# Optimization experiments

Hardware: AMD Instinct MI355X
Metric: run time of the kernel (lower is better)

The kernel has to match this reference:

```python
import jax, jax.numpy as jnp
import numpy as np

# channels_choice from the module: [8,16,24,32,40,48,56,64]
CH = jnp.arange(8, 72, 8)
EPS = 1e-5

def _masks():
    # [8,64] binary masks: mask[i, ch] = 1 if ch < channels_choice[i]
    return (jnp.arange(64)[None, :] < CH[:, None]).astype(jnp.float32)

def _bn(x, axes):
    # BatchNorm, affine=False, track_running_stats=False -> batch statistics
    mu = jnp.mean(x, axes, keepdims=True)
    var = jnp.var(x, axes, keepdims=True)
    return (x - mu) * jax.lax.rsqrt(var + EPS)

def _conv3(x, w):
    return jax.lax.conv_general_dilated(x, w, (1, 1), 'SAME',
                                        dimension_numbers=('NCHW', 'OIHW', 'NCHW'))

def _nor_conv(x, w1, w2, a1, a2):
    # Entangled two-part nor_conv edge.
    # p1: relu -> conv3x3 -> bn, mixture over 8 output-channel widths. Slicing
    # output channels + zero-pad + alpha-weighted sum collapses (BN is per-channel)
    # to a soft channel mask m1.
    masks = _masks()                      # [8,64]
    m1 = masks.T @ a1                     # [64] soft output-channel mask
    h = _bn(_conv3(jax.nn.relu(x), w1), (0, 2, 3)) * m1[None, :, None, None]
    # p2: conv3x3 -> bn, mixture over 8 input-channel widths. BN is nonlinear, so
    # the 8 candidates are genuinely computed (vectorized on a leading axis).
    xs = h[None] * masks[:, None, :, None, None]   # [8,B,64,H,W]
    K, B, C, H, W = xs.shape
    y = _conv3(xs.reshape(K * B, C, H, W), w2).reshape(K, B, C, H, W)
    y = _bn(y, (1, 3, 4))
    return jnp.einsum('k,kbchw->bchw', a2, y)

def _avg_pool3(x):
    # AvgPool2d(3, stride=1, padding=1, count_include_pad=False)
    s = jax.lax.reduce_window(x, 0.0, jax.lax.add, (1, 1, 3, 3), (1, 1, 1, 1), 'SAME')
    cnt = jax.lax.reduce_window(jnp.ones((1, 1) + x.shape[2:], x.dtype), 0.0,
                                jax.lax.add, (1, 1, 3, 3), (1, 1, 1, 1), 'SAME')
    return s / cnt

def _combi_mask(a1, a2):
    # combi=True mixture over itertools.product(channels, channels) with weights
    # a1[i]*a2[j]; for channelwise ops (skip/pool) slicing in to c_i then out to c_j
    # keeps channels < min(c_i,c_j), so the double sum factorizes into m1*m2.
    masks = _masks()
    return (masks.T @ a1) * (masks.T @ a2)

def _cell(inputs, alphas1, alphas2, W1_0, W2_0, W1_1, W2_1, W1_4, W2_4, W1_5, W2_5):
    cm = _combi_mask(alphas1, alphas2)[None, :, None, None]
    # genotype: 1<-(conv~0) | 2<-(conv~0, avgpool~1) | 3<-(skip~0, conv~1, conv~2)
    n1 = _nor_conv(inputs, W1_0, W2_0, alphas1, alphas2)
    n2 = _nor_conv(inputs, W1_1, W2_1, alphas1, alphas2) + _avg_pool3(n1) * cm
    n3 = (inputs * cm
          + _nor_conv(n1, W1_4, W2_4, alphas1, alphas2)
          + _nor_conv(n2, W1_5, W2_5, alphas1, alphas2))
    return n3

def setup_inputs():
    key = jax.random.key(0)
    ks = jax.random.split(key, 12)
    B, C, H, W = 64, 64, 32, 32
    a1 = jax.random.uniform(ks[1], (8,), jnp.float32)
    a2 = jax.random.uniform(ks[2], (8,), jnp.float32)
    d = {
        'inputs': jax.random.normal(ks[0], (B, C, H, W), jnp.float32),
        'alphas1': a1 / a1.sum(),
        'alphas2': a2 / a2.sum(),
    }
    wscale = 0.05  # ~ 1/sqrt(64*9) fan-in init
    for i, name in enumerate(['W1_0', 'W2_0', 'W1_1', 'W2_1', 'W1_4', 'W2_4', 'W1_5', 'W2_5']):
        d[name] = jax.random.normal(ks[3 + i], (64, 64, 3, 3), jnp.float32) * wscale
    return d

def reference(inputs, alphas1, alphas2, W1_0, W2_0, W1_1, W2_1, W1_4, W2_4, W1_5, W2_5):
    return _cell(inputs, alphas1, alphas2, W1_0, W2_0, W1_1, W2_1, W1_4, W2_4, W1_5, W2_5)
```

## Files before the change

### kernel.cpp

```cpp
#include <hip/hip_runtime.h>

#define EPS 1e-5f
#define NRED 65536.0f
#define IMST 73984
#define PATCH 8704

typedef short bf16x8 __attribute__((ext_vector_type(8)));
typedef float f32x4 __attribute__((ext_vector_type(4)));
typedef unsigned short u16;

#define MFMA16(a, b, c) __builtin_amdgcn_mfma_f32_16x16x32_bf16(a, b, c, 0, 0, 0)
#define SWZ(px, oct) ((px) * 64 + (((oct) ^ ((px) & 7)) * 8))

__device__ __forceinline__ u16 f2bf(float x) {
  union { float f; unsigned u; } v; v.f = x;
  unsigned r = v.u + 0x7FFF + ((v.u >> 16) & 1);
  return (u16)(r >> 16);
}
__device__ __forceinline__ float bf2f(u16 h) {
  union { unsigned u; float f; } v; v.u = ((unsigned)h) << 16;
  return v.f;
}
__device__ __forceinline__ unsigned pk2(float a, float b) {
  return (unsigned)f2bf(a) | ((unsigned)f2bf(b) << 16);
}

template <int CTRL>
__device__ __forceinline__ float dpp_mov(float x) {
  int xi = __builtin_bit_cast(int, x);
  int r = __builtin_amdgcn_update_dpp(0, xi, CTRL, 0xF, 0xF, true);
  return __builtin_bit_cast(float, r);
}
__device__ __forceinline__ float row_reduce16(float x) {
  x += dpp_mov<0x111>(x);
  x += dpp_mov<0x112>(x);
  x += dpp_mov<0x114>(x);
  x += dpp_mov<0x118>(x);
  return x;
}

__device__ __forceinline__ void stage_mask(const u16* __restrict__ src,
                                           u16* __restrict__ shp, int tid, int R0) {
#pragma unroll
  for (int i = 0; i < 5; ++i) {
    int c = i * 256 + tid;
    if (i == 4 && tid >= 64) break;
    int px = c >> 3, oct = c & 7;
    int prow = px / 34, pcol = px - prow * 34;
    bool halo = (R0 + prow == 0) || (R0 + prow == 33) || (pcol == 0) || (pcol == 33);
    uint4 v = {0u, 0u, 0u, 0u};
    if (!halo) v = *(const uint4*)&src[(size_t)c * 8];
    *(uint4*)&shp[SWZ(px, oct)] = v;
  }
}

__device__ __forceinline__ void stage_affine(const u16* __restrict__ src,
                                             u16* __restrict__ shp, int tid, int R0,
                                             const float* __restrict__ stE) {
  const int oct0 = tid & 7;
  float s[8], bb[8];
#pragma unroll
  for (int j = 0; j < 8; ++j) { s[j] = stE[oct0 * 8 + j]; bb[j] = stE[64 + oct0 * 8 + j]; }
#pragma unroll
  for (int i = 0; i < 5; ++i) {
    int c = i * 256 + tid;
    if (i == 4 && tid >= 64) break;
    int px = c >> 3, oct = c & 7;
    int prow = px / 34, pcol = px - prow * 34;
    bool halo = (R0 + prow == 0) || (R0 + prow == 33) || (pcol == 0) || (pcol == 33);
    uint4 o = {0u, 0u, 0u, 0u};
    if (!halo) {
      uint4 u = *(const uint4*)&src[(size_t)c * 8];
      unsigned uv[4] = {u.x, u.y, u.z, u.w};
      unsigned rv[4];
#pragma unroll
      for (int p2 = 0; p2 < 4; ++p2) {
        float lo = bf2f((u16)(uv[p2] & 0xffff)) * s[p2 * 2] + bb[p2 * 2];
        float hi = bf2f((u16)(uv[p2] >> 16)) * s[p2 * 2 + 1] + bb[p2 * 2 + 1];
        rv[p2] = pk2(lo, hi);
      }
      o.x = rv[0]; o.y = rv[1]; o.z = rv[2]; o.w = rv[3];
    }
    *(uint4*)&shp[SWZ(px, oct)] = o;
  }
}


__global__ void pack_wT1_k(const float* __restrict__ w0, const float* __restrict__ w1,
                           const float* __restrict__ w2, const float* __restrict__ w3,
                           u16* __restrict__ wT1) {
  int e = blockIdx.x / 9, tap = blockIdx.x % 9;
  const float* w = e == 0 ? w0 : e == 1 ? w1 : e == 2 ? w2 : w3;
  u16* dst = wT1 + e * 36864 + tap * 4096;
  for (int idx = threadIdx.x; idx < 4096; idx += 256) {
    int co = idx >> 6, ci = idx & 63;
    dst[idx] = f2bf(w[(co * 64 + ci) * 9 + tap]);
  }
}

__global__ void pack_wG_k(const float* __restrict__ w0, const float* __restrict__ w1,
                          const float* __restrict__ w2, const float* __restrict__ w3,
                          u16* __restrict__ wG64, u16* __restrict__ wT8) {
  int e = blockIdx.y;
  const float* w = e == 0 ? w0 : e == 1 ? w1 : e == 2 ? w2 : w3;
  int bx = blockIdx.x;
  int g, tap;
  u16* dst;
  if (bx < 64) { g = bx >> 3; tap = bx & 7; dst = wG64 + e * 32768 + bx * 512; }
  else         { g = bx - 64; tap = 8;      dst = wT8 + e * 4096 + g * 512; }
  for (int idx = threadIdx.x; idx < 512; idx += 256) {
    int co = idx >> 3, cig = idx & 7;
    dst[idx] = f2bf(w[(co * 64 + g * 8 + cig) * 9 + tap]);
  }
}

__global__ __launch_bounds__(256) void transpose_k(const float* __restrict__ x,
                                                   u16* __restrict__ xT) {
  __shared__ __align__(16) u16 sh[64 * 72];
  const int tid = threadIdx.x;
  const int b = blockIdx.x >> 4, slab = blockIdx.x & 15;
  const int ln = tid & 63, w = tid >> 6;
  const float* xb = x + (size_t)b * 65536 + slab * 64;
#pragma unroll
  for (int i = 0; i < 16; ++i) {
    int ci = w + i * 4;
    float v = xb[ci * 1024 + ln];
    sh[ln * 72 + ci] = f2bf(fmaxf(v, 0.f));
  }
  __syncthreads();
  u16* dst = xT + (size_t)b * IMST;
#pragma unroll
  for (int j = 0; j < 2; ++j) {
    int idx = tid + j * 256;
    int p = idx >> 3, oct = idx & 7;
    int gp = slab * 64 + p;
    int R = gp >> 5, C = gp & 31;
    *(uint4*)&dst[((R + 1) * 34 + C + 1) * 64 + oct * 8] = *(const uint4*)&sh[p * 72 + oct * 8];
  }
}

__global__ void zero_halo_k(u16* __restrict__ buf) {
  int b = blockIdx.x, tid = threadIdx.x;
  if (tid >= 132) return;
  int R, C;
  if (tid < 34) { R = 0; C = tid; }
  else if (tid < 68) { R = 33; C = tid - 34; }
  else if (tid < 100) { R = tid - 67; C = 0; }
  else { R = tid - 99; C = 33; }
  u16* p = buf + (size_t)b * IMST + (size_t)(R * 34 + C) * 64;
  uint4 z = {0u, 0u, 0u, 0u};
#pragma unroll
  for (int i = 0; i < 8; ++i) *(uint4*)&p[i * 8] = z;
}

__global__ __launch_bounds__(256, 4) void convA_k(const u16* __restrict__ in0,
                                                  const u16* __restrict__ in1,
                                                  const u16* __restrict__ wTa,
                                                  const u16* __restrict__ wTb,
                                                  u16* __restrict__ t0,
                                                  u16* __restrict__ t1,
                                                  float* __restrict__ pA) {
  __shared__ __align__(16) u16 shp[PATCH];
  __shared__ float sA[64], qA[64];
  const int tid = threadIdx.x;
  const int b = blockIdx.y, R0 = blockIdx.x * 2, z = blockIdx.z;
  const u16* xin = z ? in1 : in0;
  const u16* wT = z ? wTb : wTa;
  u16* t = z ? t1 : t0;
  if (tid < 64) { sA[tid] = 0.f; qA[tid] = 0.f; }
  stage_mask(xin + (size_t)b * IMST + (size_t)R0 * 2176, shp, tid, R0);
  const int lane = tid & 63, w = tid >> 6;
  const int ln = lane & 15, quad = lane >> 4;
  const int lr = w >> 1, mh = w & 1;
  const u16* wbase = wT + (size_t)((mh * 2) * 16 + ln) * 64 + quad * 8;
  __syncthreads();
  f32x4 acc[2][2];
#pragma unroll
  for (int m2 = 0; m2 < 2; ++m2)
#pragma unroll
    for (int nf = 0; nf < 2; ++nf) acc[m2][nf] = (f32x4){0.f, 0.f, 0.f, 0.f};
#pragma unroll 3
  for (int tap = 0; tap < 9; ++tap) {
    const int dy = tap / 3, dx = tap % 3;
    const int px0 = (lr + dy) * 34 + ln + dx;
    bf16x8 A[2][2];
#pragma unroll
    for (int m2 = 0; m2 < 2; ++m2)
#pragma unroll
      for (int h = 0; h < 2; ++h)
        A[m2][h] = *(const bf16x8*)&wbase[(size_t)(tap * 64 + m2 * 16) * 64 + h * 32];
#pragma unroll
    for (int h = 0; h < 2; ++h) {
      const int oct = h * 4 + quad;
      bf16x8 b0 = *(const bf16x8*)&shp[SWZ(px0, oct)];
      bf16x8 b1 = *(const bf16x8*)&shp[SWZ(px0 + 16, oct)];
      acc[0][0] = MFMA16(A[0][h], b0, acc[0][0]);
      acc[0][1] = MFMA16(A[0][h], b1, acc[0][1]);
      acc[1][0] = MFMA16(A[1][h], b0, acc[1][0]);
      acc[1][1] = MFMA16(A[1][h], b1, acc[1][1]);
    }
  }
  const int R = R0 + lr;
#pragma unroll
  for (int m2 = 0; m2 < 2; ++m2) {
    const int cob = (mh * 2 + m2) * 16 + quad * 4;
#pragma unroll
    for (int nf = 0; nf < 2; ++nf) {
      u16* tb = t + (size_t)b * IMST + (size_t)((R + 1) * 34 + nf * 16 + ln + 1) * 64 + cob;
      uint2 pk;
      pk.x = pk2(acc[m2][nf][0], acc[m2][nf][1]);
      pk.y = pk2(acc[m2][nf][2], acc[m2][nf][3]);
      *(uint2*)tb = pk;
    }
#pragma unroll
    for (int r = 0; r < 4; ++r) {
      float v0 = acc[m2][0][r], v1 = acc[m2][1][r];
      float s = row_reduce16(v0) + row_reduce16(v1);
      float q = row_reduce16(v0 * v0) + row_reduce16(v1 * v1);
      if (ln == 15) {
        atomicAdd(&sA[cob + r], s);
        atomicAdd(&qA[cob + r], q);
      }
    }
  }
  __syncthreads();
  const int blk = z * 1024 + blockIdx.y * 16 + blockIdx.x;
  if (tid < 64) pA[blk * 128 + tid] = sA[tid];
  else if (tid < 128) pA[blk * 128 + tid] = qA[tid - 64];
}

__global__ __launch_bounds__(256) void reducerA_k(const float* __restrict__ pA,
                                                  const float* __restrict__ a1,
                                                  float* __restrict__ stBase) {
  const int tid = threadIdx.x, c = blockIdx.x, z = blockIdx.y;
  const float* pAe = pA + (size_t)z * 1024 * 128;
  float s = 0.f, q = 0.f;
  for (int i = tid; i < 1024; i += 256) {
    s += pAe[i * 128 + c];
    q += pAe[i * 128 + 64 + c];
  }
#pragma unroll
  for (int off = 32; off; off >>= 1) { s += __shfl_xor(s, off); q += __shfl_xor(q, off); }
  __shared__ float red[8];
  int wv = tid >> 6;
  if ((tid & 63) == 0) { red[wv] = s; red[4 + wv] = q; }
  __syncthreads();
  if (tid == 0) {
    float S = red[0] + red[1] + red[2] + red[3];
    float Q = red[4] + red[5] + red[6] + red[7];
    int g = c >> 3;
    float m = 0.f;
    for (int i = g; i < 8; ++i) m += a1[i];
    float mu = S * (1.f / NRED);
    float var = Q * (1.f / NRED) - mu * mu;
    float r = rsqrtf(var + EPS);
    float* stE = stBase + z * 2048;
    stE[c] = r * m;
    stE[64 + c] = -mu * r * m;
  }
}

__global__ __launch_bounds__(256, 4) void convC_k(const u16* __restrict__ t0,
                                                  const u16* __restrict__ t1,
                                                  const u16* __restrict__ wG64,
                                                  const u16* __restrict__ wT8,
                                                  const float* __restrict__ stBase,
                                                  float* __restrict__ pC) {
  __shared__ __align__(16) u16 shp[PATCH];
  __shared__ __align__(16) u16 shA[64 * 16 * 8];
  __shared__ __align__(16) u16 shA2[8 * 16 * 8];
  __shared__ float sC[4][128], qC[4][128];
  const int tid = threadIdx.x;
  const int b = blockIdx.y, R0 = blockIdx.x * 2;
  const int edge = blockIdx.z;
  const u16* t = edge ? t1 : t0;
  const float* stE = stBase + edge * 2048;
  const u16* wGe = wG64 + edge * 32768;
  const u16* wT8e = wT8 + edge * 4096;
  {
    float* scf = (float*)sC;
    float* qcf = (float*)qC;
#pragma unroll
    for (int i = 0; i < 2; ++i) { scf[i * 256 + tid] = 0.f; qcf[i * 256 + tid] = 0.f; }
  }
  stage_affine(t + (size_t)b * IMST + (size_t)R0 * 2176, shp, tid, R0, stE);
#pragma unroll
  for (int i = 0; i < 4; ++i) {
    int c = i * 256 + tid;
    int row = c >> 4, col = c & 15;
    *(uint4*)&shA[c * 8] = *(const uint4*)&wGe[(size_t)(row * 64 + col) * 8];
  }
  if (tid < 128) {
    int g = tid >> 4, col = tid & 15;
    *(uint4*)&shA2[tid * 8] = *(const uint4*)&wT8e[(size_t)(g * 64 + col) * 8];
  }
  __syncthreads();
  const int lane = tid & 63, w = tid >> 6;
  const int ln = lane & 15, quad = lane >> 4;
  const int lrow = w >> 1, colbase = (w & 1) * 16;
  int px[3];
#pragma unroll
  for (int ch = 0; ch < 3; ++ch) {
    int tp = ch * 4 + quad; if (tp > 8) tp = 8;
    px[ch] = (lrow + tp / 3) * 34 + colbase + ln + tp % 3;
  }
#pragma unroll 1
  for (int coq = 0; coq < 4; ++coq) {
    f32x4 acc[8];
#pragma unroll
    for (int g = 0; g < 8; ++g) acc[g] = (f32x4){0.f, 0.f, 0.f, 0.f};
#pragma unroll
    for (int g = 0; g < 8; ++g) {
#pragma unroll
      for (int ch = 0; ch < 3; ++ch) {
        bf16x8 bx = *(const bf16x8*)&shp[SWZ(px[ch], g)];
        bf16x8 aw;
        if (ch < 2) {
          aw = *(const bf16x8*)&shA[((g * 8 + ch * 4 + quad) * 16 + ln) * 8];
        } else {
          aw = (bf16x8){0, 0, 0, 0, 0, 0, 0, 0};
          if (quad == 0) aw = *(const bf16x8*)&shA2[(g * 16 + ln) * 8];
        }
        acc[g] = MFMA16(aw, bx, acc[g]);
      }
    }
    f32x4 P = (f32x4){0.f, 0.f, 0.f, 0.f};
#pragma unroll
    for (int k = 0; k < 8; ++k) {
      P += acc[k];
#pragma unroll
      for (int r = 0; r < 4; ++r) {
        float v = P[r];
        float s = row_reduce16(v);
        float q = row_reduce16(v * v);
        if (ln == 15) {
          atomicAdd(&sC[coq][k * 16 + quad * 4 + r], s);
          atomicAdd(&qC[coq][k * 16 + quad * 4 + r], q);
        }
      }
    }
    __syncthreads();
    if (coq < 3) {
      const int nq = coq + 1;
#pragma unroll
      for (int i = 0; i < 4; ++i) {
        int c = i * 256 + tid;
        int row = c >> 4, col = c & 15;
        *(uint4*)&shA[c * 8] = *(const uint4*)&wGe[(size_t)(row * 64 + nq * 16 + col) * 8];
      }
      if (tid < 128) {
        int g = tid >> 4, col = tid & 15;
        *(uint4*)&shA2[tid * 8] = *(const uint4*)&wT8e[(size_t)(g * 64 + nq * 16 + col) * 8];
      }
      __syncthreads();
    }
  }
  const int blk = blockIdx.y * 16 + blockIdx.x;
#pragma unroll 1
  for (int coq = 0; coq < 4; ++coq) {
    const size_t base = ((size_t)(edge * 4 + coq) * 1024 + blk) * 256;
    if (tid < 128) pC[base + tid] = sC[coq][tid];
    else pC[base + 128 + (tid - 128)] = qC[coq][tid - 128];
  }
}

__global__ __launch_bounds__(256) void redCprepE_k(const float* __restrict__ pC,
                                                   const float* __restrict__ w2a,
                                                   const float* __restrict__ w2b,
                                                   const float* __restrict__ a1,
                                                   const float* __restrict__ a2,
                                                   float* __restrict__ stBase,
                                                   u16* __restrict__ wEbase,
                                                   float* __restrict__ cm) {
  const int tid = threadIdx.x, c = blockIdx.x, z = blockIdx.y;
  const int coq = c >> 4, cl = c & 15;
  const float* w2 = z ? w2b : w2a;
  float* stE = stBase + z * 2048;
  u16* wE = wEbase + z * 36864;
  float s[8], q[8];
#pragma unroll
  for (int k = 0; k < 8; ++k) { s[k] = 0.f; q[k] = 0.f; }
  for (int i = tid; i < 1024; i += 256) {
    const float* pb = pC + ((size_t)(z * 4 + coq) * 1024 + i) * 256;
#pragma unroll
    for (int k = 0; k < 8; ++k) {
      s[k] += pb[k * 16 + cl];
      q[k] += pb[128 + k * 16 + cl];
    }
  }
#pragma unroll
  for (int k = 0; k < 8; ++k) {
#pragma unroll
    for (int off = 32; off; off >>= 1) { s[k] += __shfl_xor(s[k], off); q[k] += __shfl_xor(q[k], off); }
  }
  __shared__ float red[4][16];
  __shared__ float gL[8];
  int wv = tid >> 6;
  if ((tid & 63) == 0) {
#pragma unroll
    for (int k = 0; k < 8; ++k) { red[wv][k * 2] = s[k]; red[wv][k * 2 + 1] = q[k]; }
  }
  __syncthreads();
  if (tid == 0) {
    float suf = 0.f, bias = 0.f;
    for (int k = 7; k >= 0; --k) {
      float S = red[0][k * 2] + red[1][k * 2] + red[2][k * 2] + red[3][k * 2];
      float Q = red[0][k * 2 + 1] + red[1][k * 2 + 1] + red[2][k * 2 + 1] + red[3][k * 2 + 1];
      float mu = S * (1.f / NRED);
      float var = Q * (1.f / NRED) - mu * mu;
      float rr = rsqrtf(var + EPS);
      bias -= a2[k] * mu * rr;
      suf += a2[k] * rr;
      gL[k] = suf;
    }
    stE[128 + c] = bias;
    if (z == 0) {
      int g = c >> 3;
      float m1 = 0.f, m2 = 0.f;
      for (int i = g; i < 8; ++i) { m1 += a1[i]; m2 += a2[i]; }
      cm[c] = m1 * m2;
    }
  }
  __syncthreads();
  for (int idx = tid; idx < 576; idx += 256) {
    int tap = idx >> 6, ci = idx & 63;
    wE[(tap * 64 + c) * 64 + ci] = f2bf(w2[(c * 64 + ci) * 9 + tap] * gL[ci >> 3]);
  }
}

template <int MODE>
__global__ __launch_bounds__(256, 4) void convE_k(const u16* __restrict__ t,
                                                  const float* __restrict__ stE,
                                                  const u16* __restrict__ wEp,
                                                  u16* __restrict__ d1,
                                                  u16* __restrict__ d2,
                                                  const float* __restrict__ cm) {
  __shared__ __align__(16) u16 shp[PATCH];
  __shared__ float cmL[64], biasL[64];
  const int tid = threadIdx.x;
  const int b = blockIdx.y, R0 = blockIdx.x * 2;
  if (tid < 64) { cmL[tid] = cm[tid]; biasL[tid] = stE[128 + tid]; }
  stage_affine(t + (size_t)b * IMST + (size_t)R0 * 2176, shp, tid, R0, stE);
  const int lane = tid & 63, w = tid >> 6;
  const int ln = lane & 15, quad = lane >> 4;
  const int lr = w >> 1, mh = w & 1;
  const u16* wbase = wEp + (size_t)((mh * 2) * 16 + ln) * 64 + quad * 8;
  __syncthreads();
  f32x4 acc[2][2];
#pragma unroll
  for (int m2 = 0; m2 < 2; ++m2)
#pragma unroll
    for (int nf = 0; nf < 2; ++nf) acc[m2][nf] = (f32x4){0.f, 0.f, 0.f, 0.f};
#pragma unroll 3
  for (int tap = 0; tap < 9; ++tap) {
    const int dy = tap / 3, dx = tap % 3;
    const int px0 = (lr + dy) * 34 + ln + dx;
    bf16x8 A[2][2];
#pragma unroll
    for (int m2 = 0; m2 < 2; ++m2)
#pragma unroll
      for (int h = 0; h < 2; ++h)
        A[m2][h] = *(const bf16x8*)&wbase[(size_t)(tap * 64 + m2 * 16) * 64 + h * 32];
#pragma unroll
    for (int h = 0; h < 2; ++h) {
      const int oct = h * 4 + quad;
      bf16x8 b0 = *(const bf16x8*)&shp[SWZ(px0, oct)];
      bf16x8 b1 = *(const bf16x8*)&shp[SWZ(px0 + 16, oct)];
      acc[0][0] = MFMA16(A[0][h], b0, acc[0][0]);
      acc[0][1] = MFMA16(A[0][h], b1, acc[0][1]);
      acc[1][0] = MFMA16(A[1][h], b0, acc[1][0]);
      acc[1][1] = MFMA16(A[1][h], b1, acc[1][1]);
    }
  }
  const int R = R0 + lr;
#pragma unroll
  for (int m2 = 0; m2 < 2; ++m2) {
    const int cob = (mh * 2 + m2) * 16 + quad * 4;
#pragma unroll
    for (int nf = 0; nf < 2; ++nf) {
      const int C = nf * 16 + ln;
      const size_t haloPx = (size_t)b * IMST + (size_t)((R + 1) * 34 + C + 1) * 64 + cob;
      float v[4];
#pragma unroll
      for (int r = 0; r < 4; ++r) v[r] = acc[m2][nf][r] + biasL[cob + r];
      if (MODE == 0) {
        uint2 pk, pkr;
        pk.x = pk2(v[0], v[1]); pk.y = pk2(v[2], v[3]);
        pkr.x = pk2(fmaxf(v[0], 0.f), fmaxf(v[1], 0.f));
        pkr.y = pk2(fmaxf(v[2], 0.f), fmaxf(v[3], 0.f));
        *(uint2*)&d1[haloPx] = pk;
        *(uint2*)&d2[haloPx] = pkr;
      } else {
        float ps[4] = {0.f, 0.f, 0.f, 0.f};
        const size_t pb2 = (size_t)b * IMST + (size_t)(R * 34 + C) * 64 + cob;
#pragma unroll
        for (int dy = 0; dy < 3; ++dy)
#pragma unroll
          for (int dx = 0; dx < 3; ++dx) {
            uint2 u = *(const uint2*)&d2[pb2 + (size_t)(dy * 34 + dx) * 64];
            ps[0] += bf2f((u16)(u.x & 0xffff));
            ps[1] += bf2f((u16)(u.x >> 16));
            ps[2] += bf2f((u16)(u.y & 0xffff));
            ps[3] += bf2f((u16)(u.y >> 16));
          }
        float rows = 3.f - (R == 0 ? 1.f : 0.f) - (R == 31 ? 1.f : 0.f);
        float cols = 3.f - (C == 0 ? 1.f : 0.f) - (C == 31 ? 1.f : 0.f);
        float inv = 1.f / (rows * cols);
        uint2 pkr;
        float t0v = fmaxf(v[0] + ps[0] * inv * cmL[cob], 0.f);
        float t1v = fmaxf(v[1] + ps[1] * inv * cmL[cob + 1], 0.f);
        float t2v = fmaxf(v[2] + ps[2] * inv * cmL[cob + 2], 0.f);
        float t3v = fmaxf(v[3] + ps[3] * inv * cmL[cob + 3], 0.f);
        pkr.x = pk2(t0v, t1v); pkr.y = pk2(t2v, t3v);
        *(uint2*)&d1[haloPx] = pkr;
      }
    }
  }
}

__global__ __launch_bounds__(256, 4) void convE23_k(const u16* __restrict__ t0,
                                                    const u16* __restrict__ t1,
                                                    const float* __restrict__ stBase,
                                                    const u16* __restrict__ wE2,
                                                    const u16* __restrict__ wE3,
                                                    float* __restrict__ outp,
                                                    const float* __restrict__ x,
                                                    const float* __restrict__ cm) {
  __shared__ __align__(16) u16 shp2[2 * PATCH];
  __shared__ float cmL[64], biasL[64];
  const int tid = threadIdx.x;
  const int b = blockIdx.y, R0 = blockIdx.x * 2;
  if (tid < 64) {
    cmL[tid] = cm[tid];
    biasL[tid] = stBase[128 + tid] + stBase[2048 + 128 + tid];
  }
  stage_affine(t0 + (size_t)b * IMST + (size_t)R0 * 2176, shp2, tid, R0, stBase);
  stage_affine(t1 + (size_t)b * IMST + (size_t)R0 * 2176, shp2 + PATCH, tid, R0, stBase + 2048);
  __syncthreads();
  const int lane = tid & 63, w = tid >> 6;
  const int ln = lane & 15, quad = lane >> 4;
  const int lr = w >> 1, mh = w & 1;
  f32x4 acc[2][2];
#pragma unroll
  for (int m2 = 0; m2 < 2; ++m2)
#pragma unroll
    for (int nf = 0; nf < 2; ++nf) acc[m2][nf] = (f32x4){0.f, 0.f, 0.f, 0.f};
#pragma unroll 1
  for (int ei = 0; ei < 2; ++ei) {
    const u16* wEp = ei ? wE3 : wE2;
    const u16* sp = &shp2[ei * PATCH];
    const u16* wbase = wEp + (size_t)((mh * 2) * 16 + ln) * 64 + quad * 8;
#pragma unroll 3
    for (int tap = 0; tap < 9; ++tap) {
      const int dy = tap / 3, dx = tap % 3;
      const int px0 = (lr + dy) * 34 + ln + dx;
      bf16x8 A[2][2];
#pragma unroll
      for (int m2 = 0; m2 < 2; ++m2)
#pragma unroll
        for (int h = 0; h < 2; ++h)
          A[m2][h] = *(const bf16x8*)&wbase[(size_t)(tap * 64 + m2 * 16) * 64 + h * 32];
#pragma unroll
      for (int h = 0; h < 2; ++h) {
        const int oct = h * 4 + quad;
        bf16x8 b0 = *(const bf16x8*)&sp[SWZ(px0, oct)];
        bf16x8 b1 = *(const bf16x8*)&sp[SWZ(px0 + 16, oct)];
        acc[0][0] = MFMA16(A[0][h], b0, acc[0][0]);
        acc[0][1] = MFMA16(A[0][h], b1, acc[0][1]);
        acc[1][0] = MFMA16(A[1][h], b0, acc[1][0]);
        acc[1][1] = MFMA16(A[1][h], b1, acc[1][1]);
      }
    }
  }
  const int R = R0 + lr;
#pragma unroll
  for (int m2 = 0; m2 < 2; ++m2) {
    const int cob = (mh * 2 + m2) * 16 + quad * 4;
#pragma unroll
    for (int nf = 0; nf < 2; ++nf) {
      const int C = nf * 16 + ln;
      size_t base = (size_t)b * 65536 + (size_t)cob * 1024 + R * 32 + C;
#pragma unroll
      for (int r = 0; r < 4; ++r)
        outp[base + (size_t)r * 1024] =
            acc[m2][nf][r] + biasL[cob + r] + x[base + (size_t)r * 1024] * cmL[cob + r];
    }
  }
}

extern "C" void kernel_launch(void* const* d_in, const int* in_sizes, int n_in,
                              void* d_out, int out_size, void* d_ws, size_t ws_size,
                              hipStream_t stream) {
  const float* x  = (const float*)d_in[0];
  const float* a1 = (const float*)d_in[1];
  const float* a2 = (const float*)d_in[2];
  const float* W1[4] = {(const float*)d_in[3], (const float*)d_in[5],
                        (const float*)d_in[7], (const float*)d_in[9]};
  const float* W2[4] = {(const float*)d_in[4], (const float*)d_in[6],
                        (const float*)d_in[8], (const float*)d_in[10]};
  float* out = (float*)d_out;
  char* ws = (char*)d_ws;
  const size_t HB = (size_t)IMST * 64 * 2;
  u16* xT  = (u16*)ws;
  u16* t0  = (u16*)(ws + HB);
  u16* t1  = (u16*)(ws + 2 * HB);
  u16* n1T = (u16*)(ws + 3 * HB);
  u16* n1r = (u16*)(ws + 4 * HB);
  u16* n2r = (u16*)(ws + 5 * HB);
  char* p = ws + 6 * HB;
  float* st  = (float*)p;            p += 8256 * 4;
  u16* wT1   = (u16*)p;              p += 4 * 36864 * 2;
  u16* wG64  = (u16*)p;              p += 4 * 32768 * 2;
  u16* wT8   = (u16*)p;              p += 4 * 4096 * 2;
  u16* wE    = (u16*)p;              p += 4 * 36864 * 2;
  float* pA  = (float*)p;            p += 2 * 1024 * 128 * 4;
  float* pC  = (float*)p;
  float* cm  = st + 8192;

  pack_wT1_k<<<36, 256, 0, stream>>>(W1[0], W1[1], W1[2], W1[3], wT1);
  pack_wG_k<<<dim3(72, 4), 256, 0, stream>>>(W2[0], W2[1], W2[2], W2[3], wG64, wT8);
  transpose_k<<<1024, 256, 0, stream>>>(x, xT);
  zero_halo_k<<<64, 160, 0, stream>>>(n1T);

  dim3 gA(16, 64, 2), gC(16, 64, 2), gE(16, 64);
  convA_k<<<gA, 256, 0, stream>>>(xT, xT, wT1, wT1 + 36864, t0, t1, pA);
  reducerA_k<<<dim3(64, 2), 256, 0, stream>>>(pA, a1, st);
  convC_k<<<gC, 256, 0, stream>>>(t0, t1, wG64, wT8, st, pC);
  redCprepE_k<<<dim3(64, 2), 256, 0, stream>>>(pC, W2[0], W2[1], a1, a2, st, wE, cm);
  convE_k<0><<<gE, 256, 0, stream>>>(t0, st, wE, n1T, n1r, cm);
  convE_k<1><<<gE, 256, 0, stream>>>(t1, st + 2048, wE + 36864, n2r, n1T, cm);
  convA_k<<<gA, 256, 0, stream>>>(n1r, n2r, wT1 + 2 * 36864, wT1 + 3 * 36864, t0, t1, pA);
  reducerA_k<<<dim3(64, 2), 256, 0, stream>>>(pA, a1, st + 4096);
  convC_k<<<gC, 256, 0, stream>>>(t0, t1, wG64 + 2 * 32768, wT8 + 2 * 4096, st + 4096, pC);
  redCprepE_k<<<dim3(64, 2), 256, 0, stream>>>(pC, W2[2], W2[3], a1, a2, st + 4096,
                                               wE + 2 * 36864, cm);
  convE23_k<<<gE, 256, 0, stream>>>(t0, t1, st + 4096, wE + 2 * 36864, wE + 3 * 36864,
                                    out, x, cm);
}
```

Baseline: 463.5 us.

## Enlarge convC tile to four rows with 512 threads and prefetch next weights

convC now runs 512-thread blocks, each covering four output rows instead of two, so every block stages a six-row patch and halves the grid. Each staged weight quarter is reused across twice as many pixels. The next output-channel quarter's weights are loaded into registers before the MFMA loop and written to shared memory afterward, hiding global load latency. The partial-stat buffer and its reducer shrink to 512 blocks per edge. The cost is higher register and LDS pressure per block, and the launch bound asks for 6 blocks of 512 threads, which may not be achievable.

Result: no change. 458.6 us (-1.1%).

```diff
diff --git a/kernel.cpp b/kernel.cpp
--- a/kernel.cpp
+++ b/kernel.cpp
@@ -4,6 +4,7 @@
 #define NRED 65536.0f
 #define IMST 73984
 #define PATCH 8704
+#define PATCH6 13056
 
 typedef short bf16x8 __attribute__((ext_vector_type(8)));
 typedef float f32x4 __attribute__((ext_vector_type(4)));
@@ -260,33 +261,57 @@
   }
 }
 
-__global__ __launch_bounds__(256, 4) void convC_k(const u16* __restrict__ t0,
+__global__ __launch_bounds__(512, 6) void convC_k(const u16* __restrict__ t0,
                                                   const u16* __restrict__ t1,
                                                   const u16* __restrict__ wG64,
                                                   const u16* __restrict__ wT8,
                                                   const float* __restrict__ stBase,
                                                   float* __restrict__ pC) {
-  __shared__ __align__(16) u16 shp[PATCH];
+  __shared__ __align__(16) u16 shp[PATCH6];
   __shared__ __align__(16) u16 shA[64 * 16 * 8];
   __shared__ __align__(16) u16 shA2[8 * 16 * 8];
   __shared__ float sC[4][128], qC[4][128];
   const int tid = threadIdx.x;
-  const int b = blockIdx.y, R0 = blockIdx.x * 2;
+  const int b = blockIdx.y, R0 = blockIdx.x * 4;
   const int edge = blockIdx.z;
   const u16* t = edge ? t1 : t0;
   const float* stE = stBase + edge * 2048;
   const u16* wGe = wG64 + edge * 32768;
   const u16* wT8e = wT8 + edge * 4096;
+  ((float*)sC)[tid] = 0.f;
+  ((float*)qC)[tid] = 0.f;
   {
-    float* scf = (float*)sC;
-    float* qcf = (float*)qC;
-#pragma unroll
-    for (int i = 0; i < 2; ++i) { scf[i * 256 + tid] = 0.f; qcf[i * 256 + tid] = 0.f; }
-  }
-  stage_affine(t + (size_t)b * IMST + (size_t)R0 * 2176, shp, tid, R0, stE);
-#pragma unroll
-  for (int i = 0; i < 4; ++i) {
-    int c = i * 256 + tid;
+    const int oct0 = tid & 7;
+    float sc[8], bc[8];
+#pragma unroll
+    for (int j = 0; j < 8; ++j) { sc[j] = stE[oct0 * 8 + j]; bc[j] = stE[64 + oct0 * 8 + j]; }
+    const u16* src = t + (size_t)b * IMST + (size_t)R0 * 2176;
+#pragma unroll
+    for (int i = 0; i < 4; ++i) {
+      int c = i * 512 + tid;
+      if (i == 3 && tid >= 96) break;
+      int px = c >> 3, oct = c & 7;
+      int prow = px / 34, pcol = px - prow * 34;
+      bool halo = (R0 + prow == 0) || (R0 + prow == 33) || (pcol == 0) || (pcol == 33);
+      uint4 o = {0u, 0u, 0u, 0u};
+      if (!halo) {
+        uint4 u = *(const uint4*)&src[(size_t)c * 8];
+        unsigned uv[4] = {u.x, u.y, u.z, u.w};
+        unsigned rv[4];
+#pragma unroll
+        for (int p2 = 0; p2 < 4; ++p2) {
+          float lo = bf2f((u16)(uv[p2] & 0xffff)) * sc[p2 * 2] + bc[p2 * 2];
+          float hi = bf2f((u16)(uv[p2] >> 16)) * sc[p2 * 2 + 1] + bc[p2 * 2 + 1];
+          rv[p2] = pk2(lo, hi);
+        }
+        o.x = rv[0]; o.y = rv[1]; o.z = rv[2]; o.w = rv[3];
+      }
+      *(uint4*)&shp[SWZ(px, oct)] = o;
+    }
+  }
+#pragma unroll
+  for (int i = 0; i < 2; ++i) {
+    int c = i * 512 + tid;
     int row = c >> 4, col = c & 15;
     *(uint4*)&shA[c * 8] = *(const uint4*)&wGe[(size_t)(row * 64 + col) * 8];
   }
@@ -306,6 +331,20 @@
   }
 #pragma unroll 1
   for (int coq = 0; coq < 4; ++coq) {
+    uint4 wr0, wr1, wr2;
+    if (coq < 3) {
+      const int nq = coq + 1;
+      {
+        int c = tid;
+        wr0 = *(const uint4*)&wGe[(size_t)((c >> 4) * 64 + nq * 16 + (c & 15)) * 8];
+      }
+      {
+        int c = 512 + tid;
+        wr1 = *(const uint4*)&wGe[(size_t)((c >> 4) * 64 + nq * 16 + (c & 15)) * 8];
+      }
+      if (tid < 128)
+        wr2 = *(const uint4*)&wT8e[(size_t)((tid >> 4) * 64 + nq * 16 + (tid & 15)) * 8];
+    }
     f32x4 acc[8];
 #pragma unroll
     for (int g = 0; g < 8; ++g) acc[g] = (f32x4){0.f, 0.f, 0.f, 0.f};
@@ -341,26 +380,19 @@
     }
     __syncthreads();
     if (coq < 3) {
-      const int nq = coq + 1;
-#pragma unroll
-      for (int i = 0; i < 4; ++i) {
-        int c = i * 256 + tid;
-        int row = c >> 4, col = c & 15;
-        *(uint4*)&shA[c * 8] = *(const uint4*)&wGe[(size_t)(row * 64 + nq * 16 + col) * 8];
-      }
-      if (tid < 128) {
-        int g = tid >> 4, col = tid & 15;
-        *(uint4*)&shA2[tid * 8] = *(const uint4*)&wT8e[(size_t)(g * 64 + nq * 16 + col) * 8];
-      }
+      *(uint4*)&shA[(size_t)tid * 8] = wr0;
+      *(uint4*)&shA[(size_t)(512 + tid) * 8] = wr1;
+      if (tid < 128) *(uint4*)&shA2[tid * 8] = wr2;
       __syncthreads();
     }
   }
-  const int blk = blockIdx.y * 16 + blockIdx.x;
+  __syncthreads();
+  const int blk = blockIdx.y * 8 + blockIdx.x;
 #pragma unroll 1
   for (int coq = 0; coq < 4; ++coq) {
-    const size_t base = ((size_t)(edge * 4 + coq) * 1024 + blk) * 256;
+    const size_t base = ((size_t)(edge * 4 + coq) * 512 + blk) * 256;
     if (tid < 128) pC[base + tid] = sC[coq][tid];
-    else pC[base + 128 + (tid - 128)] = qC[coq][tid - 128];
+    else if (tid < 256) pC[base + 128 + (tid - 128)] = qC[coq][tid - 128];
   }
 }
 
@@ -380,8 +412,8 @@
   float s[8], q[8];
 #pragma unroll
   for (int k = 0; k < 8; ++k) { s[k] = 0.f; q[k] = 0.f; }
-  for (int i = tid; i < 1024; i += 256) {
-    const float* pb = pC + ((size_t)(z * 4 + coq) * 1024 + i) * 256;
+  for (int i = tid; i < 512; i += 256) {
+    const float* pb = pC + ((size_t)(z * 4 + coq) * 512 + i) * 256;
 #pragma unroll
     for (int k = 0; k < 8; ++k) {
       s[k] += pb[k * 16 + cl];
@@ -622,16 +654,16 @@
   transpose_k<<<1024, 256, 0, stream>>>(x, xT);
   zero_halo_k<<<64, 160, 0, stream>>>(n1T);
 
-  dim3 gA(16, 64, 2), gC(16, 64, 2), gE(16, 64);
+  dim3 gA(16, 64, 2), gC(8, 64, 2), gE(16, 64);
   convA_k<<<gA, 256, 0, stream>>>(xT, xT, wT1, wT1 + 36864, t0, t1, pA);
   reducerA_k<<<dim3(64, 2), 256, 0, stream>>>(pA, a1, st);
-  convC_k<<<gC, 256, 0, stream>>>(t0, t1, wG64, wT8, st, pC);
+  convC_k<<<gC, 512, 0, stream>>>(t0, t1, wG64, wT8, st, pC);
   redCprepE_k<<<dim3(64, 2), 256, 0, stream>>>(pC, W2[0], W2[1], a1, a2, st, wE, cm);
   convE_k<0><<<gE, 256, 0, stream>>>(t0, st, wE, n1T, n1r, cm);
   convE_k<1><<<gE, 256, 0, stream>>>(t1, st + 2048, wE + 36864, n2r, n1T, cm);
   convA_k<<<gA, 256, 0, stream>>>(n1r, n2r, wT1 + 2 * 36864, wT1 + 3 * 36864, t0, t1, pA);
   reducerA_k<<<dim3(64, 2), 256, 0, stream>>>(pA, a1, st + 4096);
-  convC_k<<<gC, 256, 0, stream>>>(t0, t1, wG64 + 2 * 32768, wT8 + 2 * 4096, st + 4096, pC);
+  convC_k<<<gC, 512, 0, stream>>>(t0, t1, wG64 + 2 * 32768, wT8 + 2 * 4096, st + 4096, pC);
   redCprepE_k<<<dim3(64, 2), 256, 0, stream>>>(pC, W2[2], W2[3], a1, a2, st + 4096,
                                                wE + 2 * 36864, cm);
   convE23_k<<<gE, 256, 0, stream>>>(t0, t1, st + 4096, wE + 2 * 36864, wE + 3 * 36864,
```
